# Kernel optimization log

Hardware: AMD Instinct MI355X
Metric: run time of the kernel (lower is better)

The kernel has to match this reference:

```python
import jax, jax.numpy as jnp
import numpy as np

N_ATOMS = 10000
N_STRUCT = 100
N_PSEUDO = 4
N_SPECIES = 4
NMAX = 8
LMAX = 3
HIDDEN = 256
Q = NMAX * N_PSEUDO            # 32 radial*pseudo channels per l
N_FEAT = (LMAX + 1) * Q * Q    # 4096


def setup_inputs() -> dict:
    key = jax.random.key(0)
    ks = jax.random.split(key, 12)
    inp = {}
    for l in range(LMAX + 1):
        inp[f"c{l}"] = jax.random.normal(ks[l], (N_ATOMS, 2 * l + 1, Q), dtype=jnp.float32)
    inp["species_idx"] = jax.random.randint(ks[4], (N_ATOMS,), 0, N_SPECIES, dtype=jnp.int32)
    inp["structure_ids"] = jnp.sort(jax.random.randint(ks[5], (N_ATOMS,), 0, N_STRUCT, dtype=jnp.int32))
    inp["comb_W"] = jax.random.normal(ks[6], (N_PSEUDO, N_SPECIES), dtype=jnp.float32) / np.sqrt(N_SPECIES).astype(np.float32)
    inp["W0"] = jax.random.normal(ks[7], (N_PSEUDO, N_FEAT, HIDDEN), dtype=jnp.float32) / np.sqrt(N_FEAT).astype(np.float32)
    inp["W1"] = jax.random.normal(ks[8], (N_PSEUDO, HIDDEN, HIDDEN), dtype=jnp.float32) / np.sqrt(HIDDEN).astype(np.float32)
    inp["W2"] = jax.random.normal(ks[9], (N_PSEUDO, HIDDEN, 1), dtype=jnp.float32) / np.sqrt(HIDDEN).astype(np.float32)
    return inp


def _power_spectrum(cs):
    # Per-atom outer-product contraction over m, per angular order l.
    feats = []
    for l, c in enumerate(cs):  # c: [A, 2l+1, Q]
        cg = np.float32(1.0 / np.sqrt(2 * l + 1))
        ps = cg * jnp.einsum('amq,amr->aqr', c, c)  # [A, Q, Q]
        feats.append(ps.reshape(c.shape[0], -1))
    return jnp.concatenate(feats, axis=-1)  # [A, N_FEAT]


def reference(c0, c1, c2, c3, species_idx, structure_ids, comb_W, W0, W1, W2):
    features = _power_spectrum([c0, c1, c2, c3])  # [A, F]
    # species-gathered pseudo-species weights: one_hot(a_i) @ combination_matrix
    one_hot = jax.nn.one_hot(species_idx, N_SPECIES, dtype=features.dtype)  # [A, S]
    pw = one_hot @ comb_W.T  # [A, P]
    # embedded_features = features[:, :, None] * pw[:, None, :]
    emb = features[:, None, :] * pw[:, :, None]  # [A, P, F]
    # distinct no-bias MLP per pseudo species (SiLU activations)
    h = jax.nn.silu(jnp.einsum('apf,pfh->aph', emb, W0))
    h = jax.nn.silu(jnp.einsum('aph,phg->apg', h, W1))
    atomic = jnp.einsum('apg,pgo->apo', h, W2)[..., 0].sum(axis=1)  # [A]
    # scatter-sum atomic energies into per-structure totals (index_add_)
    energies = jax.ops.segment_sum(atomic, structure_ids, num_segments=N_STRUCT)
    return energies.reshape(-1, 1)
```

## Files before the change

### kernel.cpp

```cpp
#include <hip/hip_runtime.h>
#include <hip/hip_bf16.h>
#include <cstdint>
#include <cstddef>

#define N_ATOMS 10000
#define NSTRUCT 100
#define NP 4
#define NS 4
#define NF2 2560
#define HID 256
#define APAD 10240

#define PB_FEAT  2500
#define PB_W0    (PB_FEAT + 2560)
#define PB_W1    (PB_W0 + 256)
#define PB_ZERO  (PB_W1 + 300)
#define PB_TOTAL (PB_ZERO + 1)

typedef __attribute__((ext_vector_type(8))) _Float16 f16x8;
typedef __attribute__((ext_vector_type(8))) ushort u16x8;
typedef __attribute__((ext_vector_type(4))) float f32x4;

__device__ __forceinline__ float silu(float x) {
  return x / (1.f + __expf(-x));
}
__device__ __forceinline__ ushort f2h(float x) {
  _Float16 h = (_Float16)x;
  return *reinterpret_cast<ushort*>(&h);
}
__device__ __forceinline__ void cdec(int c, int& q, int& b) {
  if (c < 32)      { q = c >> 2; b = c & 3; }
  else if (c < 56) { int x = c - 32; int j = (x * 171) >> 9; q = 8 + j; b = 1 + (x - j * 3); }
  else if (c < 72) { int x = c - 56; q = 16 + (x >> 1); b = 2 + (x & 1); }
  else             { q = 24 + (c - 72); b = 3; }
}

typedef __attribute__((address_space(3))) uint32_t lds_u32;
typedef const __attribute__((address_space(1))) uint32_t glb_u32;
__device__ __forceinline__ void glds16(const ushort* g, ushort* l) {
  __builtin_amdgcn_global_load_lds((glb_u32*)g, (lds_u32*)l, 16, 0, 0);
}

__global__ __launch_bounds__(256) void prep_kernel(
    const float* __restrict__ c0, const float* __restrict__ c1,
    const float* __restrict__ c2, const float* __restrict__ c3,
    const float* __restrict__ W0, const float* __restrict__ W1,
    ushort* __restrict__ fh, ushort* __restrict__ W0t,
    ushort* __restrict__ W1t, float* __restrict__ out) {
  __shared__ float shbuf[2048];
  int b = blockIdx.x;
  int tid = threadIdx.x;

  if (b < PB_FEAT) {
    int wv = tid >> 6, lane = tid & 63;
    int a = b * 4 + wv;
    float* cs = shbuf + wv * 512;
    for (int i = 0; i < 8; ++i) {
      int e = lane + i * 64;
      float v;
      if (e < 32)       v = c0[a * 32  + e];
      else if (e < 128) v = c1[a * 96  + (e - 32)];
      else if (e < 288) v = c2[a * 160 + (e - 128)];
      else              v = c3[a * 224 + (e - 288)];
      cs[e] = v;
    }
    __syncthreads();
    const float cg[4]  = {1.0f, 0.5773502691896258f, 0.4472135954999579f, 0.3779644730092272f};
    const int  off[4]  = {0, 32, 128, 288};
    const int  nm[4]   = {1, 3, 5, 7};
#pragma unroll
    for (int t = 0; t < 5; ++t) {
      int cc = lane + t * 64;
      int l = cc / 80, c = cc - l * 80;
      int q, bb; cdec(c, q, bb);
      int rb = bb * 8;
      const float* base = cs + off[l];
      float s[8] = {0.f, 0.f, 0.f, 0.f, 0.f, 0.f, 0.f, 0.f};
      for (int m = 0; m < nm[l]; ++m) {
        float bq = base[m * 32 + q];
        float4 v0 = *reinterpret_cast<const float4*>(&base[m * 32 + rb]);
        float4 v1 = *reinterpret_cast<const float4*>(&base[m * 32 + rb + 4]);
        s[0] += bq * v0.x; s[1] += bq * v0.y; s[2] += bq * v0.z; s[3] += bq * v0.w;
        s[4] += bq * v1.x; s[5] += bq * v1.y; s[6] += bq * v1.z; s[7] += bq * v1.w;
      }
      u16x8 o;
#pragma unroll
      for (int u = 0; u < 8; ++u) o[u] = f2h(s[u] * cg[l]);
      *reinterpret_cast<u16x8*>(&fh[(size_t)a * NF2 + cc * 8]) = o;
    }
  } else if (b < PB_W0) {
    int idx = b - PB_FEAT;
    int nx = idx & 7;
    int rest = idx >> 3;
    int ky = rest % 80, p = rest / 80;
    int kt = ky * 32, nt = nx * 32;
    int lx = tid & 31, ly = tid >> 5;
    float (*t)[33] = (float(*)[33])shbuf;
    const float* src = W0 + (size_t)p * 4096 * HID;
#pragma unroll
    for (int i = 0; i < 4; ++i) {
      int kf = kt + ly + i * 8;
      int l = kf / 640, w = kf - l * 640;
      int c = w >> 3, s = w & 7;
      int q, bb; cdec(c, q, bb);
      int r = bb * 8 + s;
      float v = 0.f;
      if (r >= q) {
        v = src[(size_t)(l * 1024 + q * 32 + r) * HID + nt + lx];
        if (r > q) v += src[(size_t)(l * 1024 + r * 32 + q) * HID + nt + lx];
      }
      t[ly + i * 8][lx] = v;
    }
    __syncthreads();
    ushort* dst = W0t + (size_t)p * HID * NF2;
#pragma unroll
    for (int i = 0; i < 4; ++i)
      dst[(size_t)(nt + ly + i * 8) * NF2 + kt + lx] = f2h(t[lx][ly + i * 8]);
  } else if (b < PB_W1) {
    int idx = b - PB_W0;
    int nx = idx & 7, ky = (idx >> 3) & 7, p = idx >> 6;
    int kt = ky * 32, nt = nx * 32;
    int lx = tid & 31, ly = tid >> 5;
    float (*t)[33] = (float(*)[33])shbuf;
    const float* src = W1 + (size_t)p * HID * HID;
#pragma unroll
    for (int i = 0; i < 4; ++i)
      t[ly + i * 8][lx] = src[(size_t)(kt + ly + i * 8) * HID + nt + lx];
    __syncthreads();
    ushort* dst = W1t + (size_t)p * HID * HID;
#pragma unroll
    for (int i = 0; i < 4; ++i)
      dst[(size_t)(nt + ly + i * 8) * HID + kt + lx] = f2h(t[lx][ly + i * 8]);
  } else if (b < PB_ZERO) {
    int idx = b - PB_W1;
    size_t e = (size_t)idx * 2048 + tid * 8;
    u16x8 z = (u16x8){0, 0, 0, 0, 0, 0, 0, 0};
    *reinterpret_cast<u16x8*>(&fh[(size_t)N_ATOMS * NF2 + e]) = z;
  } else {
    if (tid < NSTRUCT) out[tid] = 0.f;
  }
}

__global__ __launch_bounds__(256) void gemm0_mfma(
    const ushort* __restrict__ fh, const ushort* __restrict__ W0t,
    const float* __restrict__ combW, const int* __restrict__ species,
    ushort* __restrict__ h0f) {
  __shared__ ushort As[64 * 64];
  __shared__ ushort Bs[64 * 64];
  int tid = threadIdx.x;
  int linear = blockIdx.y * 8 + blockIdx.x;
  int xc = linear & 7, sq = linear >> 3;
  int bm = ((sq >> 3) * 8 + xc) * 128;
  int bn = (sq & 7) * 128;
  int wid = tid >> 6, lane = tid & 63;
  int wm = (wid >> 1) * 64, wn = (wid & 1) * 64;
  int mh = wid >> 1, nh = wid & 1;

  int pr = tid >> 3, pc = tid & 7;
  int lg = pc ^ (pr & 7);
  int mhalf = lg >> 2, kc = lg & 3;
  const ushort* gaA1 = fh  + ((size_t)(bm + pr + 64 * mhalf) * NF2 + kc * 8);
  const ushort* gaA2 = gaA1 + (size_t)32 * NF2;
  const ushort* gaB1 = W0t + ((size_t)(bn + pr + 64 * mhalf) * NF2 + kc * 8);
  const ushort* gaB2 = gaB1 + (size_t)32 * NF2;
  ushort* lA = As + tid * 8;
  ushort* lB = Bs + tid * 8;

  f32x4 acc[4][4];
#pragma unroll
  for (int i = 0; i < 4; ++i)
#pragma unroll
    for (int j = 0; j < 4; ++j) acc[i][j] = (f32x4){0.f, 0.f, 0.f, 0.f};

  int mrow = lane & 15;
  int h7 = mrow & 7;
  int qv = lane >> 4;
  int pcA = ((mh << 2) | qv) ^ h7;
  int pcB = ((nh << 2) | qv) ^ h7;

  for (int k0 = 0; k0 < NF2; k0 += 32) {
    glds16(gaA1 + k0, lA);
    glds16(gaA2 + k0, lA + 2048);
    glds16(gaB1 + k0, lB);
    glds16(gaB2 + k0, lB + 2048);
    __syncthreads();

    f16x8 af[4], bf[4];
#pragma unroll
    for (int i = 0; i < 4; ++i) {
      af[i] = *reinterpret_cast<const f16x8*>(&As[(i * 16 + mrow) * 64 + pcA * 8]);
      bf[i] = *reinterpret_cast<const f16x8*>(&Bs[(i * 16 + mrow) * 64 + pcB * 8]);
    }
#pragma unroll
    for (int i = 0; i < 4; ++i)
#pragma unroll
      for (int j = 0; j < 4; ++j)
        acc[i][j] = __builtin_amdgcn_mfma_f32_16x16x32_f16(af[i], bf[j], acc[i][j], 0, 0, 0);
    __syncthreads();
  }

  int p = bn >> 8;
  int col = lane & 15, rbase = (lane >> 4) * 4;
#pragma unroll
  for (int i = 0; i < 4; ++i) {
#pragma unroll
    for (int r = 0; r < 4; ++r) {
      int m = bm + wm + i * 16 + rbase + r;
      bool live = (m < N_ATOMS);
      float pw = live ? combW[p * NS + species[m]] : 0.f;
#pragma unroll
      for (int j = 0; j < 4; ++j) {
        int n = bn + wn + j * 16 + col;
        float v = live ? silu(pw * acc[i][j][r]) : 0.f;
        h0f[(size_t)m * 1024 + n] = f2h(v);
      }
    }
  }
}

__global__ __launch_bounds__(256) void mlp1_mfma(
    const ushort* __restrict__ h0f, const ushort* __restrict__ W1t,
    const float* __restrict__ W2, const int* __restrict__ sid,
    float* __restrict__ out) {
  __shared__ ushort As[64 * 256];
  __shared__ float sout[NSTRUCT];
  int tid = threadIdx.x;
  int linear = blockIdx.x;
  int xc = linear & 7, s = linear >> 3;
  int p = s & 3, t = s >> 2;
  int bm = ((t >> 1) * 8 + xc) * 128 + (t & 1) * 64;
  int wid = tid >> 6, lane = tid & 63;
  int wn = wid * 64;

  if (tid < NSTRUCT) sout[tid] = 0.f;

  int mrow = lane & 15;
  int qv = lane >> 4;
  int h7 = mrow & 7;

#pragma unroll
  for (int s8 = 0; s8 < 8; ++s8) {
    int d = s8 * 256 + tid;
    int r = d >> 5, pcs = d & 31;
    int lc = pcs ^ (r & 7);
    glds16(h0f + (size_t)(bm + r) * 1024 + p * 256 + lc * 8, As + d * 8);
  }

  const ushort* wb = W1t + (size_t)p * HID * HID;
  const ushort* wrow[4];
#pragma unroll
  for (int j = 0; j < 4; ++j)
    wrow[j] = wb + (size_t)(wn + j * 16 + mrow) * 256 + qv * 8;

  f16x8 bc[4], bn_[4];
#pragma unroll
  for (int j = 0; j < 4; ++j) bc[j] = *reinterpret_cast<const f16x8*>(wrow[j]);

  __syncthreads();

  f32x4 acc[4][4];
#pragma unroll
  for (int i = 0; i < 4; ++i)
#pragma unroll
    for (int j = 0; j < 4; ++j) acc[i][j] = (f32x4){0.f, 0.f, 0.f, 0.f};

#pragma unroll
  for (int ki = 0; ki < 8; ++ki) {
    if (ki < 7) {
#pragma unroll
      for (int j = 0; j < 4; ++j)
        bn_[j] = *reinterpret_cast<const f16x8*>(wrow[j] + (ki + 1) * 32);
    }
    f16x8 af[4];
#pragma unroll
    for (int i = 0; i < 4; ++i) {
      int row = i * 16 + mrow;
      int pc2 = (ki * 4 + qv) ^ h7;
      af[i] = *reinterpret_cast<const f16x8*>(&As[row * 256 + pc2 * 8]);
    }
#pragma unroll
    for (int i = 0; i < 4; ++i)
#pragma unroll
      for (int j = 0; j < 4; ++j)
        acc[i][j] = __builtin_amdgcn_mfma_f32_16x16x32_f16(af[i], bc[j], acc[i][j], 0, 0, 0);
    if (ki < 7) {
#pragma unroll
      for (int j = 0; j < 4; ++j) bc[j] = bn_[j];
    }
  }

  int col = lane & 15, quad = lane >> 4;
  float w2j[4];
#pragma unroll
  for (int j = 0; j < 4; ++j) w2j[j] = W2[p * 256 + wn + j * 16 + col];
  float runv = 0.f;
  int runs = -1;
#pragma unroll
  for (int i = 0; i < 4; ++i) {
#pragma unroll
    for (int r = 0; r < 4; ++r) {
      float v = silu(acc[i][0][r]) * w2j[0] + silu(acc[i][1][r]) * w2j[1]
              + silu(acc[i][2][r]) * w2j[2] + silu(acc[i][3][r]) * w2j[3];
      v += __shfl_xor(v, 1, 64);
      v += __shfl_xor(v, 2, 64);
      v += __shfl_xor(v, 4, 64);
      v += __shfl_xor(v, 8, 64);
      if (col == 0) {
        int m = bm + i * 16 + quad * 4 + r;
        int s_ = (m < N_ATOMS) ? sid[m] : -1;
        if (s_ != runs) {
          if (runs >= 0) atomicAdd(&sout[runs], runv);
          runs = s_;
          runv = 0.f;
        }
        if (s_ >= 0) runv += v;
      }
    }
  }
  if (col == 0 && runs >= 0) atomicAdd(&sout[runs], runv);

  __syncthreads();
  if (tid < NSTRUCT) {
    float v = sout[tid];
    if (v != 0.f) atomicAdd(&out[tid], v);
  }
}

extern "C" void kernel_launch(void* const* d_in, const int* in_sizes, int n_in,
                              void* d_out, int out_size, void* d_ws, size_t ws_size,
                              hipStream_t stream) {
  const float* c0      = (const float*)d_in[0];
  const float* c1      = (const float*)d_in[1];
  const float* c2      = (const float*)d_in[2];
  const float* c3      = (const float*)d_in[3];
  const int*   species = (const int*)d_in[4];
  const int*   sid     = (const int*)d_in[5];
  const float* combW   = (const float*)d_in[6];
  const float* W0      = (const float*)d_in[7];
  const float* W1      = (const float*)d_in[8];
  const float* W2      = (const float*)d_in[9];
  float*       out     = (float*)d_out;

  ushort* fh  = (ushort*)d_ws;
  ushort* W0t = fh  + (size_t)APAD * NF2;
  ushort* W1t = W0t + (size_t)NP * HID * NF2;
  ushort* h0f = W1t + (size_t)NP * HID * HID;

  prep_kernel<<<PB_TOTAL, 256, 0, stream>>>(c0, c1, c2, c3, W0, W1,
                                            fh, W0t, W1t, out);

  dim3 g2(8, APAD / 128);
  gemm0_mfma<<<g2, 256, 0, stream>>>(fh, W0t, combW, species, h0f);

  mlp1_mfma<<<640, 256, 0, stream>>>(h0f, W1t, W2, sid, out);
}
```

Before: 199.3 us.

## Replace LDS-staged GEMM0 with direct global-to-register loads and register double buffering

The first-layer GEMM no longer stages A/B tiles through shared memory with barriers. Each wave now loads its MFMA fragments straight from global memory into registers, using two register buffers so the next k-slice loads while the current one is multiplied. The block shrinks to 128 threads computing 128x64 tiles, and blocks are remapped over a 1D grid of 1280 for XCD-aware scheduling. This removes LDS traffic and syncs, but drops cross-wave reuse of tiles, so it relies on L2/L1 for reuse and issues many more uncoalesced 16-byte global loads.

```diff
diff --git a/kernel.cpp b/kernel.cpp
--- a/kernel.cpp
+++ b/kernel.cpp
@@ -141,30 +141,27 @@
   }
 }
 
-__global__ __launch_bounds__(256) void gemm0_mfma(
+__global__ __launch_bounds__(128) void gemm0_mfma(
     const ushort* __restrict__ fh, const ushort* __restrict__ W0t,
     const float* __restrict__ combW, const int* __restrict__ species,
     ushort* __restrict__ h0f) {
-  __shared__ ushort As[64 * 64];
-  __shared__ ushort Bs[64 * 64];
   int tid = threadIdx.x;
-  int linear = blockIdx.y * 8 + blockIdx.x;
-  int xc = linear & 7, sq = linear >> 3;
-  int bm = ((sq >> 3) * 8 + xc) * 128;
-  int bn = (sq & 7) * 128;
+  int orig = blockIdx.x;
+  int wgid = (orig & 7) * 160 + (orig >> 3);
+  int bm = (wgid >> 4) * 128;
+  int bn = (wgid & 15) * 64;
   int wid = tid >> 6, lane = tid & 63;
-  int wm = (wid >> 1) * 64, wn = (wid & 1) * 64;
-  int mh = wid >> 1, nh = wid & 1;
-
-  int pr = tid >> 3, pc = tid & 7;
-  int lg = pc ^ (pr & 7);
-  int mhalf = lg >> 2, kc = lg & 3;
-  const ushort* gaA1 = fh  + ((size_t)(bm + pr + 64 * mhalf) * NF2 + kc * 8);
-  const ushort* gaA2 = gaA1 + (size_t)32 * NF2;
-  const ushort* gaB1 = W0t + ((size_t)(bn + pr + 64 * mhalf) * NF2 + kc * 8);
-  const ushort* gaB2 = gaB1 + (size_t)32 * NF2;
-  ushort* lA = As + tid * 8;
-  ushort* lB = Bs + tid * 8;
+  int wm = wid * 64;
+  int mrow = lane & 15, qv = lane >> 4;
+
+  const ushort* pA[4];
+  const ushort* pB[4];
+#pragma unroll
+  for (int i = 0; i < 4; ++i)
+    pA[i] = fh + (size_t)(bm + wm + i * 16 + mrow) * NF2 + qv * 8;
+#pragma unroll
+  for (int j = 0; j < 4; ++j)
+    pB[j] = W0t + (size_t)(bn + j * 16 + mrow) * NF2 + qv * 8;
 
   f32x4 acc[4][4];
 #pragma unroll
@@ -172,31 +169,34 @@
 #pragma unroll
     for (int j = 0; j < 4; ++j) acc[i][j] = (f32x4){0.f, 0.f, 0.f, 0.f};
 
-  int mrow = lane & 15;
-  int h7 = mrow & 7;
-  int qv = lane >> 4;
-  int pcA = ((mh << 2) | qv) ^ h7;
-  int pcB = ((nh << 2) | qv) ^ h7;
-
-  for (int k0 = 0; k0 < NF2; k0 += 32) {
-    glds16(gaA1 + k0, lA);
-    glds16(gaA2 + k0, lA + 2048);
-    glds16(gaB1 + k0, lB);
-    glds16(gaB2 + k0, lB + 2048);
-    __syncthreads();
-
-    f16x8 af[4], bf[4];
+  f16x8 a0[4], b0[4], a1[4], b1[4];
+#pragma unroll
+  for (int i = 0; i < 4; ++i) {
+    a0[i] = *reinterpret_cast<const f16x8*>(pA[i]);
+    b0[i] = *reinterpret_cast<const f16x8*>(pB[i]);
+  }
+
+  for (int k0 = 0; k0 < NF2; k0 += 64) {
 #pragma unroll
     for (int i = 0; i < 4; ++i) {
-      af[i] = *reinterpret_cast<const f16x8*>(&As[(i * 16 + mrow) * 64 + pcA * 8]);
-      bf[i] = *reinterpret_cast<const f16x8*>(&Bs[(i * 16 + mrow) * 64 + pcB * 8]);
+      a1[i] = *reinterpret_cast<const f16x8*>(pA[i] + k0 + 32);
+      b1[i] = *reinterpret_cast<const f16x8*>(pB[i] + k0 + 32);
     }
 #pragma unroll
     for (int i = 0; i < 4; ++i)
 #pragma unroll
       for (int j = 0; j < 4; ++j)
-        acc[i][j] = __builtin_amdgcn_mfma_f32_16x16x32_f16(af[i], bf[j], acc[i][j], 0, 0, 0);
-    __syncthreads();
+        acc[i][j] = __builtin_amdgcn_mfma_f32_16x16x32_f16(a0[i], b0[j], acc[i][j], 0, 0, 0);
+#pragma unroll
+    for (int i = 0; i < 4; ++i) {
+      a0[i] = *reinterpret_cast<const f16x8*>(pA[i] + k0 + 64);
+      b0[i] = *reinterpret_cast<const f16x8*>(pB[i] + k0 + 64);
+    }
+#pragma unroll
+    for (int i = 0; i < 4; ++i)
+#pragma unroll
+      for (int j = 0; j < 4; ++j)
+        acc[i][j] = __builtin_amdgcn_mfma_f32_16x16x32_f16(a1[i], b1[j], acc[i][j], 0, 0, 0);
   }
 
   int p = bn >> 8;
@@ -210,7 +210,7 @@
       float pw = live ? combW[p * NS + species[m]] : 0.f;
 #pragma unroll
       for (int j = 0; j < 4; ++j) {
-        int n = bn + wn + j * 16 + col;
+        int n = bn + j * 16 + col;
         float v = live ? silu(pw * acc[i][j][r]) : 0.f;
         h0f[(size_t)m * 1024 + n] = f2h(v);
       }
@@ -349,8 +349,7 @@
   prep_kernel<<<PB_TOTAL, 256, 0, stream>>>(c0, c1, c2, c3, W0, W1,
                                             fh, W0t, W1t, out);
 
-  dim3 g2(8, APAD / 128);
-  gemm0_mfma<<<g2, 256, 0, stream>>>(fh, W0t, combW, species, h0f);
+  gemm0_mfma<<<1280, 128, 0, stream>>>(fh, W0t, combW, species, h0f);
 
   mlp1_mfma<<<640, 256, 0, stream>>>(h0f, W1t, W2, sid, out);
 }
```

New measurement: 358.7 us. +80.0%, slower.

## Pre-swizzle W0 into MFMA fragment layout and load B directly to registers

Applied to the files above, without the earlier changes.

The W0 transpose pre-pass now writes weights in a fragment-tiled layout so each lane can load its MFMA B operand with one contiguous 16-byte global read. The gemm0 kernel drops the shared-memory B tile and double-buffers B fragments in registers across two K-steps, so the B global loads overlap the MFMA work. This cuts LDS traffic and LDS footprint for B. In exchange, each wave reads B from global/L2 separately with no sharing through LDS, register pressure rises, and the loop still synchronises twice per K-step for the A tile.

```diff
diff --git a/kernel.cpp b/kernel.cpp
--- a/kernel.cpp
+++ b/kernel.cpp
@@ -114,8 +114,11 @@
     __syncthreads();
     ushort* dst = W0t + (size_t)p * HID * NF2;
 #pragma unroll
-    for (int i = 0; i < 4; ++i)
-      dst[(size_t)(nt + ly + i * 8) * NF2 + kt + lx] = f2h(t[lx][ly + i * 8]);
+    for (int i = 0; i < 4; ++i) {
+      int h = nt + ly + i * 8;
+      int off = ((h >> 4) * 80 + ky) * 512 + (h & 15) * 8 + (lx >> 3) * 128 + (lx & 7);
+      dst[off] = f2h(t[lx][ly + i * 8]);
+    }
   } else if (b < PB_W1) {
     int idx = b - PB_W0;
     int nx = idx & 7, ky = (idx >> 3) & 7, p = idx >> 6;
@@ -146,7 +149,6 @@
     const float* __restrict__ combW, const int* __restrict__ species,
     ushort* __restrict__ h0f) {
   __shared__ ushort As[64 * 64];
-  __shared__ ushort Bs[64 * 64];
   int tid = threadIdx.x;
   int linear = blockIdx.y * 8 + blockIdx.x;
   int xc = linear & 7, sq = linear >> 3;
@@ -154,17 +156,19 @@
   int bn = (sq & 7) * 128;
   int wid = tid >> 6, lane = tid & 63;
   int wm = (wid >> 1) * 64, wn = (wid & 1) * 64;
-  int mh = wid >> 1, nh = wid & 1;
+  int mh = wid >> 1;
 
   int pr = tid >> 3, pc = tid & 7;
   int lg = pc ^ (pr & 7);
   int mhalf = lg >> 2, kc = lg & 3;
   const ushort* gaA1 = fh  + ((size_t)(bm + pr + 64 * mhalf) * NF2 + kc * 8);
   const ushort* gaA2 = gaA1 + (size_t)32 * NF2;
-  const ushort* gaB1 = W0t + ((size_t)(bn + pr + 64 * mhalf) * NF2 + kc * 8);
-  const ushort* gaB2 = gaB1 + (size_t)32 * NF2;
   ushort* lA = As + tid * 8;
-  ushort* lB = Bs + tid * 8;
+
+  int p = bn >> 8;
+  int hh0 = (bn & 255) + wn;
+  const ushort* pBb = W0t + (size_t)p * HID * NF2
+                    + (size_t)(hh0 >> 4) * 80 * 512 + lane * 8;
 
   f32x4 acc[4][4];
 #pragma unroll
@@ -176,30 +180,54 @@
   int h7 = mrow & 7;
   int qv = lane >> 4;
   int pcA = ((mh << 2) | qv) ^ h7;
-  int pcB = ((nh << 2) | qv) ^ h7;
-
-  for (int k0 = 0; k0 < NF2; k0 += 32) {
-    glds16(gaA1 + k0, lA);
-    glds16(gaA2 + k0, lA + 2048);
-    glds16(gaB1 + k0, lB);
-    glds16(gaB2 + k0, lB + 2048);
-    __syncthreads();
-
-    f16x8 af[4], bf[4];
-#pragma unroll
-    for (int i = 0; i < 4; ++i) {
-      af[i] = *reinterpret_cast<const f16x8*>(&As[(i * 16 + mrow) * 64 + pcA * 8]);
-      bf[i] = *reinterpret_cast<const f16x8*>(&Bs[(i * 16 + mrow) * 64 + pcB * 8]);
-    }
-#pragma unroll
-    for (int i = 0; i < 4; ++i)
+
+  f16x8 bA[4], bB[4];
+#pragma unroll
+  for (int j = 0; j < 4; ++j)
+    bA[j] = *reinterpret_cast<const f16x8*>(pBb + j * 40960);
+
+  const int NK = NF2 / 32;
+  for (int t = 0; t < NK; t += 2) {
+    glds16(gaA1 + t * 32, lA);
+    glds16(gaA2 + t * 32, lA + 2048);
+#pragma unroll
+    for (int j = 0; j < 4; ++j)
+      bB[j] = *reinterpret_cast<const f16x8*>(pBb + j * 40960 + (t + 1) * 512);
+    __syncthreads();
+    {
+      f16x8 af[4];
+#pragma unroll
+      for (int i = 0; i < 4; ++i)
+        af[i] = *reinterpret_cast<const f16x8*>(&As[(i * 16 + mrow) * 64 + pcA * 8]);
+#pragma unroll
+      for (int i = 0; i < 4; ++i)
+#pragma unroll
+        for (int j = 0; j < 4; ++j)
+          acc[i][j] = __builtin_amdgcn_mfma_f32_16x16x32_f16(af[i], bA[j], acc[i][j], 0, 0, 0);
+    }
+    __syncthreads();
+    glds16(gaA1 + (t + 1) * 32, lA);
+    glds16(gaA2 + (t + 1) * 32, lA + 2048);
+    if (t + 2 < NK) {
 #pragma unroll
       for (int j = 0; j < 4; ++j)
-        acc[i][j] = __builtin_amdgcn_mfma_f32_16x16x32_f16(af[i], bf[j], acc[i][j], 0, 0, 0);
-    __syncthreads();
-  }
-
-  int p = bn >> 8;
+        bA[j] = *reinterpret_cast<const f16x8*>(pBb + j * 40960 + (t + 2) * 512);
+    }
+    __syncthreads();
+    {
+      f16x8 af[4];
+#pragma unroll
+      for (int i = 0; i < 4; ++i)
+        af[i] = *reinterpret_cast<const f16x8*>(&As[(i * 16 + mrow) * 64 + pcA * 8]);
+#pragma unroll
+      for (int i = 0; i < 4; ++i)
+#pragma unroll
+        for (int j = 0; j < 4; ++j)
+          acc[i][j] = __builtin_amdgcn_mfma_f32_16x16x32_f16(af[i], bB[j], acc[i][j], 0, 0, 0);
+    }
+    __syncthreads();
+  }
+
   int col = lane & 15, rbase = (lane >> 4) * 4;
 #pragma unroll
   for (int i = 0; i < 4; ++i) {
```

After: 205.5 us. 1.03x slower.

## Fuse layer-0 GEMM with layer-1 MLP, keeping hidden activations in LDS

Applied to the files above, without the earlier changes.

Merges the first-layer GEMM and the second-layer MLP/reduction into one kernel. Each block computes a 64x256 hidden tile for one pseudo species, applies SiLU and stores it swizzled in shared memory, then runs the W1 GEMM and the W2 reduction directly. This removes the global write and read of the intermediate activations and one kernel launch. In exchange, the layer-0 tile becomes 64x256, so more W0 data is streamed per FLOP and each atom tile is loaded once per pseudo species.

```diff
diff --git a/kernel.cpp b/kernel.cpp
--- a/kernel.cpp
+++ b/kernel.cpp
@@ -141,88 +141,12 @@
   }
 }
 
-__global__ __launch_bounds__(256) void gemm0_mfma(
+__global__ __launch_bounds__(256) void gemm_fused(
     const ushort* __restrict__ fh, const ushort* __restrict__ W0t,
     const float* __restrict__ combW, const int* __restrict__ species,
-    ushort* __restrict__ h0f) {
-  __shared__ ushort As[64 * 64];
-  __shared__ ushort Bs[64 * 64];
-  int tid = threadIdx.x;
-  int linear = blockIdx.y * 8 + blockIdx.x;
-  int xc = linear & 7, sq = linear >> 3;
-  int bm = ((sq >> 3) * 8 + xc) * 128;
-  int bn = (sq & 7) * 128;
-  int wid = tid >> 6, lane = tid & 63;
-  int wm = (wid >> 1) * 64, wn = (wid & 1) * 64;
-  int mh = wid >> 1, nh = wid & 1;
-
-  int pr = tid >> 3, pc = tid & 7;
-  int lg = pc ^ (pr & 7);
-  int mhalf = lg >> 2, kc = lg & 3;
-  const ushort* gaA1 = fh  + ((size_t)(bm + pr + 64 * mhalf) * NF2 + kc * 8);
-  const ushort* gaA2 = gaA1 + (size_t)32 * NF2;
-  const ushort* gaB1 = W0t + ((size_t)(bn + pr + 64 * mhalf) * NF2 + kc * 8);
-  const ushort* gaB2 = gaB1 + (size_t)32 * NF2;
-  ushort* lA = As + tid * 8;
-  ushort* lB = Bs + tid * 8;
-
-  f32x4 acc[4][4];
-#pragma unroll
-  for (int i = 0; i < 4; ++i)
-#pragma unroll
-    for (int j = 0; j < 4; ++j) acc[i][j] = (f32x4){0.f, 0.f, 0.f, 0.f};
-
-  int mrow = lane & 15;
-  int h7 = mrow & 7;
-  int qv = lane >> 4;
-  int pcA = ((mh << 2) | qv) ^ h7;
-  int pcB = ((nh << 2) | qv) ^ h7;
-
-  for (int k0 = 0; k0 < NF2; k0 += 32) {
-    glds16(gaA1 + k0, lA);
-    glds16(gaA2 + k0, lA + 2048);
-    glds16(gaB1 + k0, lB);
-    glds16(gaB2 + k0, lB + 2048);
-    __syncthreads();
-
-    f16x8 af[4], bf[4];
-#pragma unroll
-    for (int i = 0; i < 4; ++i) {
-      af[i] = *reinterpret_cast<const f16x8*>(&As[(i * 16 + mrow) * 64 + pcA * 8]);
-      bf[i] = *reinterpret_cast<const f16x8*>(&Bs[(i * 16 + mrow) * 64 + pcB * 8]);
-    }
-#pragma unroll
-    for (int i = 0; i < 4; ++i)
-#pragma unroll
-      for (int j = 0; j < 4; ++j)
-        acc[i][j] = __builtin_amdgcn_mfma_f32_16x16x32_f16(af[i], bf[j], acc[i][j], 0, 0, 0);
-    __syncthreads();
-  }
-
-  int p = bn >> 8;
-  int col = lane & 15, rbase = (lane >> 4) * 4;
-#pragma unroll
-  for (int i = 0; i < 4; ++i) {
-#pragma unroll
-    for (int r = 0; r < 4; ++r) {
-      int m = bm + wm + i * 16 + rbase + r;
-      bool live = (m < N_ATOMS);
-      float pw = live ? combW[p * NS + species[m]] : 0.f;
-#pragma unroll
-      for (int j = 0; j < 4; ++j) {
-        int n = bn + wn + j * 16 + col;
-        float v = live ? silu(pw * acc[i][j][r]) : 0.f;
-        h0f[(size_t)m * 1024 + n] = f2h(v);
-      }
-    }
-  }
-}
-
-__global__ __launch_bounds__(256) void mlp1_mfma(
-    const ushort* __restrict__ h0f, const ushort* __restrict__ W1t,
-    const float* __restrict__ W2, const int* __restrict__ sid,
-    float* __restrict__ out) {
-  __shared__ ushort As[64 * 256];
+    const ushort* __restrict__ W1t, const float* __restrict__ W2,
+    const int* __restrict__ sid, float* __restrict__ out) {
+  __shared__ ushort sh[16384];
   __shared__ float sout[NSTRUCT];
   int tid = threadIdx.x;
   int linear = blockIdx.x;
@@ -234,17 +158,76 @@
 
   if (tid < NSTRUCT) sout[tid] = 0.f;
 
-  int mrow = lane & 15;
-  int qv = lane >> 4;
-  int h7 = mrow & 7;
-
-#pragma unroll
-  for (int s8 = 0; s8 < 8; ++s8) {
-    int d = s8 * 256 + tid;
-    int r = d >> 5, pcs = d & 31;
-    int lc = pcs ^ (r & 7);
-    glds16(h0f + (size_t)(bm + r) * 1024 + p * 256 + lc * 8, As + d * 8);
-  }
+  int mrow = lane & 15, qv = lane >> 4, h7 = mrow & 7;
+
+  {
+  }
+  int prA = tid >> 3, pcA_ = tid & 7;
+  int lgA = pcA_ ^ (prA & 7);
+  const ushort* gA = fh + (size_t)(bm + prA + 32 * (lgA >> 2)) * NF2 + (lgA & 3) * 8;
+  ushort* lA = sh + tid * 8;
+  int prB = tid >> 3, pcB_ = tid & 7;
+  int lgB = pcB_ ^ (prB & 7);
+  int mhB = lgB >> 2, kcB = lgB & 3;
+  const ushort* wp = W0t + (size_t)p * HID * NF2;
+  const ushort* gB0 = wp + (size_t)(prB +  0 + 128 * mhB) * NF2 + kcB * 8;
+  const ushort* gB1 = wp + (size_t)(prB + 32 + 128 * mhB) * NF2 + kcB * 8;
+  const ushort* gB2 = wp + (size_t)(prB + 64 + 128 * mhB) * NF2 + kcB * 8;
+  const ushort* gB3 = wp + (size_t)(prB + 96 + 128 * mhB) * NF2 + kcB * 8;
+  ushort* lB = sh + 2048 + tid * 8;
+
+  f32x4 acc[4][4];
+#pragma unroll
+  for (int i = 0; i < 4; ++i)
+#pragma unroll
+    for (int j = 0; j < 4; ++j) acc[i][j] = (f32x4){0.f, 0.f, 0.f, 0.f};
+
+  int pcB = ((wid >> 1) * 4 + qv) ^ h7;
+  int browb = (wid & 1) * 64;
+
+  for (int k0 = 0; k0 < NF2; k0 += 32) {
+    glds16(gA  + k0, lA);
+    glds16(gB0 + k0, lB);
+    glds16(gB1 + k0, lB + 2048);
+    glds16(gB2 + k0, lB + 4096);
+    glds16(gB3 + k0, lB + 6144);
+    __syncthreads();
+
+    f16x8 af[4], bf[4];
+#pragma unroll
+    for (int i = 0; i < 4; ++i) {
+      int pca = ((i >> 1) * 4 + qv) ^ h7;
+      af[i] = *reinterpret_cast<const f16x8*>(&sh[((i & 1) * 16 + mrow) * 64 + pca * 8]);
+    }
+#pragma unroll
+    for (int j = 0; j < 4; ++j)
+      bf[j] = *reinterpret_cast<const f16x8*>(&sh[2048 + (browb + j * 16 + mrow) * 64 + pcB * 8]);
+#pragma unroll
+    for (int i = 0; i < 4; ++i)
+#pragma unroll
+      for (int j = 0; j < 4; ++j)
+        acc[i][j] = __builtin_amdgcn_mfma_f32_16x16x32_f16(af[i], bf[j], acc[i][j], 0, 0, 0);
+    __syncthreads();
+  }
+
+  int col = lane & 15, quad = lane >> 4;
+#pragma unroll
+  for (int i = 0; i < 4; ++i) {
+#pragma unroll
+    for (int r = 0; r < 4; ++r) {
+      int mloc = i * 16 + quad * 4 + r;
+      int m = bm + mloc;
+      bool live = (m < N_ATOMS);
+      float pw = live ? combW[p * NS + species[m]] : 0.f;
+#pragma unroll
+      for (int j = 0; j < 4; ++j) {
+        int h = wn + j * 16 + col;
+        float v = live ? silu(pw * acc[i][j][r]) : 0.f;
+        sh[mloc * 256 + (((h >> 3) ^ (mloc & 7)) << 3) + (h & 7)] = f2h(v);
+      }
+    }
+  }
+  __syncthreads();
 
   const ushort* wb = W1t + (size_t)p * HID * HID;
   const ushort* wrow[4];
@@ -256,13 +239,11 @@
 #pragma unroll
   for (int j = 0; j < 4; ++j) bc[j] = *reinterpret_cast<const f16x8*>(wrow[j]);
 
-  __syncthreads();
-
-  f32x4 acc[4][4];
+  f32x4 acc2[4][4];
 #pragma unroll
   for (int i = 0; i < 4; ++i)
 #pragma unroll
-    for (int j = 0; j < 4; ++j) acc[i][j] = (f32x4){0.f, 0.f, 0.f, 0.f};
+    for (int j = 0; j < 4; ++j) acc2[i][j] = (f32x4){0.f, 0.f, 0.f, 0.f};
 
 #pragma unroll
   for (int ki = 0; ki < 8; ++ki) {
@@ -276,20 +257,19 @@
     for (int i = 0; i < 4; ++i) {
       int row = i * 16 + mrow;
       int pc2 = (ki * 4 + qv) ^ h7;
-      af[i] = *reinterpret_cast<const f16x8*>(&As[row * 256 + pc2 * 8]);
+      af[i] = *reinterpret_cast<const f16x8*>(&sh[row * 256 + pc2 * 8]);
     }
 #pragma unroll
     for (int i = 0; i < 4; ++i)
 #pragma unroll
       for (int j = 0; j < 4; ++j)
-        acc[i][j] = __builtin_amdgcn_mfma_f32_16x16x32_f16(af[i], bc[j], acc[i][j], 0, 0, 0);
+        acc2[i][j] = __builtin_amdgcn_mfma_f32_16x16x32_f16(af[i], bc[j], acc2[i][j], 0, 0, 0);
     if (ki < 7) {
 #pragma unroll
       for (int j = 0; j < 4; ++j) bc[j] = bn_[j];
     }
   }
 
-  int col = lane & 15, quad = lane >> 4;
   float w2j[4];
 #pragma unroll
   for (int j = 0; j < 4; ++j) w2j[j] = W2[p * 256 + wn + j * 16 + col];
@@ -299,8 +279,8 @@
   for (int i = 0; i < 4; ++i) {
 #pragma unroll
     for (int r = 0; r < 4; ++r) {
-      float v = silu(acc[i][0][r]) * w2j[0] + silu(acc[i][1][r]) * w2j[1]
-              + silu(acc[i][2][r]) * w2j[2] + silu(acc[i][3][r]) * w2j[3];
+      float v = silu(acc2[i][0][r]) * w2j[0] + silu(acc2[i][1][r]) * w2j[1]
+              + silu(acc2[i][2][r]) * w2j[2] + silu(acc2[i][3][r]) * w2j[3];
       v += __shfl_xor(v, 1, 64);
       v += __shfl_xor(v, 2, 64);
       v += __shfl_xor(v, 4, 64);
@@ -344,13 +324,10 @@
   ushort* fh  = (ushort*)d_ws;
   ushort* W0t = fh  + (size_t)APAD * NF2;
   ushort* W1t = W0t + (size_t)NP * HID * NF2;
-  ushort* h0f = W1t + (size_t)NP * HID * HID;
 
   prep_kernel<<<PB_TOTAL, 256, 0, stream>>>(c0, c1, c2, c3, W0, W1,
                                             fh, W0t, W1t, out);
 
-  dim3 g2(8, APAD / 128);
-  gemm0_mfma<<<g2, 256, 0, stream>>>(fh, W0t, combW, species, h0f);
-
-  mlp1_mfma<<<640, 256, 0, stream>>>(h0f, W1t, W2, sid, out);
-}
+  gemm_fused<<<640, 256, 0, stream>>>(fh, W0t, combW, species,
+                                      W1t, W2, sid, out);
+}
```

Measured after the change: 252.4 us. 1.27x slower.
